# Kernel optimization log

Measured on AMD Instinct MI355X. Metric: run time of the kernel, lower is better.

The kernel has to match this reference:

```python
import jax, jax.numpy as jnp
import numpy as np

DIM = 288          # = C*9 patch features
RED = DIM // 2     # 144, reduced dim inside EffAttention
HEADS = 8
HD = RED // HEADS  # 18
SCALE = HD ** -0.5
NCHUNK = 4
EPS = 1e-5


def layer_norm(x, g, b):
    mu = jnp.mean(x, axis=-1, keepdims=True)
    var = jnp.mean(jnp.square(x - mu), axis=-1, keepdims=True)
    return (x - mu) * jax.lax.rsqrt(var + EPS) * g + b


def extract_patches_3x3(x):
    # x: [B, C, H, W] -> [B, C*9, H*W], same padding, stride 1.
    # Channel ordering matches torch.nn.Unfold: index = c*9 + ki*3 + kj.
    B, C, H, W = x.shape
    xp = jnp.pad(x, ((0, 0), (0, 0), (1, 1), (1, 1)))
    pats = jnp.stack([xp[:, :, i:i + H, j:j + W]
                      for i in range(3) for j in range(3)], axis=2)  # [B,C,9,H,W]
    return pats.reshape(B, C * 9, H * W)


def eff_attention(x, reduce_w, qkv_w, proj_w, proj_b):
    # x: [B, N, DIM]
    B, N, _ = x.shape
    h = x @ reduce_w                                   # [B, N, RED]
    qkv = (h @ qkv_w).reshape(B, N, 3, HEADS, HD)
    qkv = qkv.transpose(2, 0, 3, 1, 4)                 # [3, B, H, N, hd]
    q, k, v = qkv[0], qkv[1], qkv[2]
    chunk = N // NCHUNK
    q = q.reshape(B, HEADS, NCHUNK, chunk, HD)
    k = k.reshape(B, HEADS, NCHUNK, chunk, HD)
    v = v.reshape(B, HEADS, NCHUNK, chunk, HD)
    attn = jnp.einsum('bhcqd,bhckd->bhcqk', q, k) * SCALE
    attn = jax.nn.softmax(attn, axis=-1)
    out = jnp.einsum('bhcqk,bhckd->bhcqd', attn, v)    # [B,H,c,q,hd]
    out = out.transpose(0, 2, 3, 1, 4).reshape(B, N, RED)
    return out @ proj_w + proj_b


def setup_inputs() -> dict:
    key = jax.random.key(0)
    ks = jax.random.split(key, 12)
    s = 0.05
    return {
        'x': jax.random.normal(ks[0], (4, 32, 64, 64), jnp.float32),
        'norm1_g': jnp.ones((DIM,), jnp.float32),
        'norm1_b': jnp.zeros((DIM,), jnp.float32),
        'reduce_w': jax.random.normal(ks[1], (DIM, RED), jnp.float32) * s,
        'qkv_w': jax.random.normal(ks[2], (RED, 3 * RED), jnp.float32) * s,
        'proj_w': jax.random.normal(ks[3], (RED, DIM), jnp.float32) * s,
        'proj_b': jnp.zeros((DIM,), jnp.float32),
        'norm2_g': jnp.ones((DIM,), jnp.float32),
        'norm2_b': jnp.zeros((DIM,), jnp.float32),
        'fc1_w': jax.random.normal(ks[4], (DIM, DIM // 4), jnp.float32) * s,
        'fc1_b': jnp.zeros((DIM // 4,), jnp.float32),
        'fc2_w': jax.random.normal(ks[5], (DIM // 4, DIM), jnp.float32) * s,
        'fc2_b': jnp.zeros((DIM,), jnp.float32),
    }


def reference(x, norm1_g, norm1_b, reduce_w, qkv_w, proj_w, proj_b,
              norm2_g, norm2_b, fc1_w, fc1_b, fc2_w, fc2_b):
    t = extract_patches_3x3(x).transpose(0, 2, 1)      # [B, N, DIM]
    t = t + eff_attention(layer_norm(t, norm1_g, norm1_b),
                          reduce_w, qkv_w, proj_w, proj_b)
    h = layer_norm(t, norm2_g, norm2_b)
    h = jax.nn.relu(h @ fc1_w + fc1_b) @ fc2_w + fc2_b
    return t + h
```

## Files before the change

kernel.cpp:

```cpp
#include <hip/hip_runtime.h>
#include <hip/hip_bf16.h>

typedef __attribute__((ext_vector_type(4))) float f32x4;
typedef __attribute__((ext_vector_type(8))) short s16x8;
typedef __attribute__((ext_vector_type(2))) unsigned int u32x2;
typedef __attribute__((ext_vector_type(4))) unsigned int u32x4;
typedef unsigned short u16;
typedef unsigned int u32;

#define MTOT 16384
#define QSCALE 0.34004649151f

__device__ __forceinline__ u16 f2bf(float f){
  u32 u = __builtin_bit_cast(u32, f);
  u = (u + 0x7fffu + ((u >> 16) & 1u)) >> 16;
  return (u16)u;
}
__device__ __forceinline__ float bf2f(u16 u){
  u32 x = ((u32)u) << 16;
  return __builtin_bit_cast(float, x);
}
__device__ __forceinline__ float bfu32lo(u32 w){ return __builtin_bit_cast(float, (u32)(w << 16)); }
__device__ __forceinline__ float bfu32hi(u32 w){ return __builtin_bit_cast(float, (u32)(w & 0xffff0000u)); }
__device__ __forceinline__ u32 cvtpk(float lo, float hi){
  u32 r;
  asm("v_cvt_pk_bf16_f32 %0, %1, %2" : "=v"(r) : "v"(lo), "v"(hi));
  return r;
}
__device__ __forceinline__ float fexp2(float x){
  float r;
  asm("v_exp_f32 %0, %1" : "=v"(r) : "v"(x));
  return r;
}

__global__ __launch_bounds__(256) void head_k(
    const float* __restrict__ x, const float* __restrict__ g, const float* __restrict__ b_,
    u16* __restrict__ tb, u16* __restrict__ ln1,
    const float* __restrict__ rw, const float* __restrict__ qw,
    const float* __restrict__ pw, const float* __restrict__ f1, const float* __restrict__ f2,
    u16* __restrict__ WcT, u16* __restrict__ pwT, u16* __restrict__ f1wT, u16* __restrict__ f2wT)
{
  __shared__ float lds_t[32][296];
  __shared__ float red_s[8][32];
  __shared__ float red_q[8][32];
  __shared__ float smu[32], srs[32];
  int bid = blockIdx.x;
  int tid = threadIdx.x;
  if (bid >= 512){
    int idx = (bid - 512) * 256 + tid;
    const int N1 = 288*432, N2 = 288*160, N3 = 72*288;
    if (idx < N1){
      int i = idx / 432, j = idx - i * 432;
      float acc = 0.f;
      for (int k = 0; k < 144; ++k) acc += rw[i*144 + k] * qw[k*432 + j];
      WcT[j*288 + i] = f2bf(acc);
    } else if (idx < N1 + N2){
      int t = idx - N1; int n = t / 160, k = t - n * 160;
      pwT[t] = (k < 144) ? f2bf(pw[k*288 + n]) : (u16)0;
    } else if (idx < N1 + N2 + N3){
      int t = idx - (N1 + N2); int n = t / 288, k = t - n * 288;
      f1wT[t] = f2bf(f1[k*72 + n]);
    } else {
      int t = idx - (N1 + N2 + N3); int n = t / 96, k = t - n * 96;
      f2wT[t] = (k < 72) ? f2bf(f2[k*288 + n]) : (u16)0;
    }
    return;
  }
  int b = bid >> 7, i = (bid >> 1) & 63, j0 = (bid & 1) * 32;
  int q = tid >> 5;
  int jl = tid & 31;
  int j = j0 + jl;
  const float* xb = x + ((long)b * 32) * 4096;
  float s = 0.f, ss = 0.f;
#pragma unroll
  for (int c4 = 0; c4 < 4; ++c4){
    int c = q * 4 + c4;
    const float* xc = xb + c * 4096;
#pragma unroll
    for (int di = 0; di < 3; ++di){
      int ii = i + di - 1;
      bool iok = (ii >= 0) && (ii < 64);
#pragma unroll
      for (int dj = 0; dj < 3; ++dj){
        int jj = j + dj - 1;
        float v = 0.f;
        if (iok && jj >= 0 && jj < 64) v = xc[ii * 64 + jj];
        lds_t[jl][c * 9 + di * 3 + dj] = v;
        s += v; ss += v * v;
      }
    }
  }
  red_s[q][jl] = s; red_q[q][jl] = ss;
  __syncthreads();
  if (q == 0){
    float S = 0.f, SS = 0.f;
#pragma unroll
    for (int k = 0; k < 8; ++k){ S += red_s[k][jl]; SS += red_q[k][jl]; }
    float mu = S * (1.f/288.f);
    float var = SS * (1.f/288.f) - mu * mu;
    smu[jl] = mu;
    srs[jl] = rsqrtf(var + 1e-5f);
  }
  __syncthreads();
  long rowbase = ((long)b * 4096 + i * 64 + j0) * 288;
  for (int it = 0; it < 9; ++it){
    int idx = tid + it * 256;
    int p = idx / 72;
    int kk = idx - p * 72;
    f32x4 v = *(f32x4*)&lds_t[p][kk * 4];
    long base = rowbase + (long)p * 288 + kk * 4;
    u32x2 pt;
    pt[0] = (u32)f2bf(v[0]) | ((u32)f2bf(v[1]) << 16);
    pt[1] = (u32)f2bf(v[2]) | ((u32)f2bf(v[3]) << 16);
    *(u32x2*)&tb[base] = pt;
    float mu = smu[p], rs = srs[p];
    u16 o0 = f2bf((v[0]-mu)*rs*g[kk*4+0] + b_[kk*4+0]);
    u16 o1 = f2bf((v[1]-mu)*rs*g[kk*4+1] + b_[kk*4+1]);
    u16 o2 = f2bf((v[2]-mu)*rs*g[kk*4+2] + b_[kk*4+2]);
    u16 o3 = f2bf((v[3]-mu)*rs*g[kk*4+3] + b_[kk*4+3]);
    u32x2 pk;
    pk[0] = (u32)o0 | ((u32)o1 << 16);
    pk[1] = (u32)o2 | ((u32)o3 << 16);
    *(u32x2*)&ln1[base] = pk;
  }
}

template<int MODE, int KP, int MR>
__global__ __launch_bounds__(256) void gemm_k(
    const u16* __restrict__ A, const u16* __restrict__ BT,
    const float* __restrict__ bias, const void* __restrict__ resp,
    void* __restrict__ out0, void* __restrict__ out1, void* __restrict__ out2,
    int M, int N, int K)
{
  __shared__ u16 As[MR][KP + 8];
  __shared__ u16 Bs[64][KP + 8];
  const int nseg = KP >> 3;
  int tid = threadIdx.x;
  int m0 = blockIdx.x * MR, n0 = blockIdx.y * 64;
  for (int idx = tid; idx < (MR + 64) * nseg; idx += 256){
    int r = idx / nseg, sg = idx - r * nseg;
    if (r < MR){
      s16x8 v = {0,0,0,0,0,0,0,0};
      if (sg * 8 < K) v = *(const s16x8*)(A + (long)(m0 + r) * K + sg * 8);
      *(s16x8*)&As[r][sg * 8] = v;
    } else {
      int rb = r - MR;
      s16x8 w = {0,0,0,0,0,0,0,0};
      if (n0 + rb < N) w = *(const s16x8*)(BT + (long)(n0 + rb) * KP + sg * 8);
      *(s16x8*)&Bs[rb][sg * 8] = w;
    }
  }
  __syncthreads();
  int wv = tid >> 6, l = tid & 63;
  int lq = l & 15, lg = l >> 4;

#define EPI(ACC, MROW, NCOL) {                                           \
    int mrow = (MROW);                                                   \
    int ncol = (NCOL);                                                   \
    if (ncol < N){                                                       \
      if (MODE == 0){                                                    \
        int which = ncol / 144;                                          \
        int rem = ncol - which * 144;                                    \
        int hh = rem / 18;                                               \
        int dd = rem - hh * 18;                                          \
        _Pragma("unroll")                                                \
        for (int e = 0; e < 4; ++e){                                     \
          int row = mrow + e;                                            \
          long bch = (long)((row >> 10) * 8 + hh);                       \
          int kk = row & 1023;                                           \
          float v = ACC[e];                                              \
          if (which == 0){                                               \
            ((u16*)out0)[(bch<<15) + kk*32 + dd] = f2bf(v * QSCALE);     \
            if (dd < 14) ((u16*)out0)[(bch<<15) + kk*32 + 18 + dd] = (u16)0; \
          } else if (which == 1){                                        \
            int cp = (dd >> 3) ^ ((kk >> 1) & 3);                        \
            ((u16*)out1)[(bch<<15) + kk*32 + (cp<<3) + (dd&7)] = f2bf(v);\
          } else {                                                       \
            int seg = kk >> 8, jg = (kk >> 3) & 31, jp = jg ^ (dd & 7);  \
            ((u16*)out2)[(bch<<15) + seg*8192 + dd*256 + (jp<<3) + (kk&7)] = f2bf(v); \
            if (dd == 0){                                                \
              int jp1 = jg ^ 2;                                          \
              ((u16*)out2)[(bch<<15) + seg*8192 + 18*256 + (jp1<<3) + (kk&7)] = (u16)0x3F80; \
            }                                                            \
          }                                                              \
        }                                                                \
      } else {                                                           \
        float bv = bias[ncol];                                           \
        _Pragma("unroll")                                                \
        for (int e = 0; e < 4; ++e){                                     \
          long off = (long)(mrow + e) * N + ncol;                        \
          float v = ACC[e] + bv;                                         \
          if (MODE == 1){ v += bf2f(((const u16*)resp)[off]); ((u16*)out0)[off] = f2bf(v); } \
        }                                                                \
      }                                                                  \
    }                                                                    \
  }

  if constexpr (MR == 64){
    int wr = wv >> 1, wc = wv & 1;
    f32x4 acc00={0,0,0,0}, acc01={0,0,0,0}, acc10={0,0,0,0}, acc11={0,0,0,0};
    for (int kt = 0; kt < KP; kt += 32){
      s16x8 a0 = *(const s16x8*)&As[wr*32 + lq][kt + lg*8];
      s16x8 a1 = *(const s16x8*)&As[wr*32 + 16 + lq][kt + lg*8];
      s16x8 b0 = *(const s16x8*)&Bs[wc*32 + lq][kt + lg*8];
      s16x8 b1 = *(const s16x8*)&Bs[wc*32 + 16 + lq][kt + lg*8];
      acc00 = __builtin_amdgcn_mfma_f32_16x16x32_bf16(a0, b0, acc00, 0, 0, 0);
      acc01 = __builtin_amdgcn_mfma_f32_16x16x32_bf16(a0, b1, acc01, 0, 0, 0);
      acc10 = __builtin_amdgcn_mfma_f32_16x16x32_bf16(a1, b0, acc10, 0, 0, 0);
      acc11 = __builtin_amdgcn_mfma_f32_16x16x32_bf16(a1, b1, acc11, 0, 0, 0);
    }
    EPI(acc00, m0 + wr*32 + 0*16 + lg*4, n0 + wc*32 + 0*16 + lq)
    EPI(acc01, m0 + wr*32 + 0*16 + lg*4, n0 + wc*32 + 1*16 + lq)
    EPI(acc10, m0 + wr*32 + 1*16 + lg*4, n0 + wc*32 + 0*16 + lq)
    EPI(acc11, m0 + wr*32 + 1*16 + lg*4, n0 + wc*32 + 1*16 + lq)
  } else {
    f32x4 c00={0,0,0,0}, c01={0,0,0,0}, c02={0,0,0,0}, c03={0,0,0,0};
    f32x4 c10={0,0,0,0}, c11={0,0,0,0}, c12={0,0,0,0}, c13={0,0,0,0};
    for (int kt = 0; kt < KP; kt += 32){
      s16x8 a0 = *(const s16x8*)&As[wv*32 + lq][kt + lg*8];
      s16x8 a1 = *(const s16x8*)&As[wv*32 + 16 + lq][kt + lg*8];
      s16x8 b0 = *(const s16x8*)&Bs[ 0 + lq][kt + lg*8];
      s16x8 b1 = *(const s16x8*)&Bs[16 + lq][kt + lg*8];
      s16x8 b2 = *(const s16x8*)&Bs[32 + lq][kt + lg*8];
      s16x8 b3 = *(const s16x8*)&Bs[48 + lq][kt + lg*8];
      c00 = __builtin_amdgcn_mfma_f32_16x16x32_bf16(a0, b0, c00, 0, 0, 0);
      c01 = __builtin_amdgcn_mfma_f32_16x16x32_bf16(a0, b1, c01, 0, 0, 0);
      c02 = __builtin_amdgcn_mfma_f32_16x16x32_bf16(a0, b2, c02, 0, 0, 0);
      c03 = __builtin_amdgcn_mfma_f32_16x16x32_bf16(a0, b3, c03, 0, 0, 0);
      c10 = __builtin_amdgcn_mfma_f32_16x16x32_bf16(a1, b0, c10, 0, 0, 0);
      c11 = __builtin_amdgcn_mfma_f32_16x16x32_bf16(a1, b1, c11, 0, 0, 0);
      c12 = __builtin_amdgcn_mfma_f32_16x16x32_bf16(a1, b2, c12, 0, 0, 0);
      c13 = __builtin_amdgcn_mfma_f32_16x16x32_bf16(a1, b3, c13, 0, 0, 0);
    }
    EPI(c00, m0 + wv*32 + lg*4,      n0 +  0 + lq)
    EPI(c01, m0 + wv*32 + lg*4,      n0 + 16 + lq)
    EPI(c02, m0 + wv*32 + lg*4,      n0 + 32 + lq)
    EPI(c03, m0 + wv*32 + lg*4,      n0 + 48 + lq)
    EPI(c10, m0 + wv*32 + 16 + lg*4, n0 +  0 + lq)
    EPI(c11, m0 + wv*32 + 16 + lg*4, n0 + 16 + lq)
    EPI(c12, m0 + wv*32 + 16 + lg*4, n0 + 32 + lq)
    EPI(c13, m0 + wv*32 + 16 + lg*4, n0 + 48 + lq)
  }
#undef EPI
}

__global__ __launch_bounds__(256) void attn_k(
    const u16* __restrict__ Qp, const u16* __restrict__ Kpp,
    const u16* __restrict__ Vt, u16* __restrict__ ao)
{
  __shared__ u16 Ks[8192];
  __shared__ u16 Vs[8192];
  int bid = blockIdx.x;
  int qt = bid >> 7, bch = bid & 127;
  int b = bch >> 5, c = (bch >> 3) & 3, h = bch & 7;
  int tid = threadIdx.x, wv = tid >> 6, l = tid & 63;
  int lq = l & 15, lg = l >> 4;
  long base = (long)bch << 15;
  int q0 = qt * 256 + wv * 64 + lq;
  s16x8 qf0 = *(const s16x8*)(Qp + base + (long)(q0     ) * 32 + lg * 8);
  s16x8 qf1 = *(const s16x8*)(Qp + base + (long)(q0 + 16) * 32 + lg * 8);
  s16x8 qf2 = *(const s16x8*)(Qp + base + (long)(q0 + 32) * 32 + lg * 8);
  s16x8 qf3 = *(const s16x8*)(Qp + base + (long)(q0 + 48) * 32 + lg * 8);
  f32x4 oA0={0,0,0,0}, oA1={0,0,0,0}, oA2={0,0,0,0}, oA3={0,0,0,0};
  f32x4 oB0={0,0,0,0}, oB1={0,0,0,0}, oB2={0,0,0,0}, oB3={0,0,0,0};
  const f32x4 zf = {0,0,0,0};
  const u16* kg = Kpp + base;
  const u16* vg = Vt + base;
  u32x4 kr[4], vr[4];
#pragma unroll
  for (int r = 0; r < 4; ++r){
    kr[r] = *(const u32x4*)(kg + (r*256 + tid) * 8);
    vr[r] = *(const u32x4*)(vg + (r*256 + tid) * 8);
  }
  int kswz = (lq >> 1) & 3;
  int vswz = lq & 7;
  int ho = (lg & 1) << 2;
  int gl = lg >> 1;
  for (int seg = 0; seg < 4; ++seg){
    __syncthreads();
#pragma unroll
    for (int r = 0; r < 4; ++r){
      *(u32x4*)&Ks[(r*256 + tid) * 8] = kr[r];
      *(u32x4*)&Vs[(r*256 + tid) * 8] = vr[r];
    }
    __syncthreads();
    if (seg < 3){
      const u16* kgn = kg + (seg + 1) * 8192;
      const u16* vgn = vg + (seg + 1) * 8192;
#pragma unroll
      for (int r = 0; r < 4; ++r){
        kr[r] = *(const u32x4*)(kgn + (r*256 + tid) * 8);
        vr[r] = *(const u32x4*)(vgn + (r*256 + tid) * 8);
      }
    }
#pragma unroll 2
    for (int t32 = 0; t32 < 8; ++t32){
      int k0 = t32 * 32;
      int r0 = k0 + lq, r1 = k0 + 16 + lq;
      s16x8 kf0 = *(const s16x8*)&Ks[r0*32 + ((lg ^ kswz) << 3)];
      s16x8 kf1 = *(const s16x8*)&Ks[r1*32 + ((lg ^ kswz) << 3)];
      f32x4 s00 = __builtin_amdgcn_mfma_f32_16x16x32_bf16(kf0, qf0, zf, 0, 0, 0);
      f32x4 s01 = __builtin_amdgcn_mfma_f32_16x16x32_bf16(kf0, qf1, zf, 0, 0, 0);
      f32x4 s02 = __builtin_amdgcn_mfma_f32_16x16x32_bf16(kf0, qf2, zf, 0, 0, 0);
      f32x4 s03 = __builtin_amdgcn_mfma_f32_16x16x32_bf16(kf0, qf3, zf, 0, 0, 0);
      f32x4 s10 = __builtin_amdgcn_mfma_f32_16x16x32_bf16(kf1, qf0, zf, 0, 0, 0);
      f32x4 s11 = __builtin_amdgcn_mfma_f32_16x16x32_bf16(kf1, qf1, zf, 0, 0, 0);
      f32x4 s12 = __builtin_amdgcn_mfma_f32_16x16x32_bf16(kf1, qf2, zf, 0, 0, 0);
      f32x4 s13 = __builtin_amdgcn_mfma_f32_16x16x32_bf16(kf1, qf3, zf, 0, 0, 0);
      s16x8 pb0, pb1, pb2, pb3;
      {
        u32x4 w0, w1, w2, w3;
        w0[0] = cvtpk(fexp2(s00[0]), fexp2(s00[1]));
        w0[1] = cvtpk(fexp2(s00[2]), fexp2(s00[3]));
        w0[2] = cvtpk(fexp2(s10[0]), fexp2(s10[1]));
        w0[3] = cvtpk(fexp2(s10[2]), fexp2(s10[3]));
        w1[0] = cvtpk(fexp2(s01[0]), fexp2(s01[1]));
        w1[1] = cvtpk(fexp2(s01[2]), fexp2(s01[3]));
        w1[2] = cvtpk(fexp2(s11[0]), fexp2(s11[1]));
        w1[3] = cvtpk(fexp2(s11[2]), fexp2(s11[3]));
        w2[0] = cvtpk(fexp2(s02[0]), fexp2(s02[1]));
        w2[1] = cvtpk(fexp2(s02[2]), fexp2(s02[3]));
        w2[2] = cvtpk(fexp2(s12[0]), fexp2(s12[1]));
        w2[3] = cvtpk(fexp2(s12[2]), fexp2(s12[3]));
        w3[0] = cvtpk(fexp2(s03[0]), fexp2(s03[1]));
        w3[1] = cvtpk(fexp2(s03[2]), fexp2(s03[3]));
        w3[2] = cvtpk(fexp2(s13[0]), fexp2(s13[1]));
        w3[3] = cvtpk(fexp2(s13[2]), fexp2(s13[3]));
        pb0 = __builtin_bit_cast(s16x8, w0);
        pb1 = __builtin_bit_cast(s16x8, w1);
        pb2 = __builtin_bit_cast(s16x8, w2);
        pb3 = __builtin_bit_cast(s16x8, w3);
      }
      int G1 = (k0 >> 3) + gl;
      int a_lo = lq*256 + ((G1 ^ vswz) << 3) + ho;
      int a_hi = lq*256 + (((G1 + 2) ^ vswz) << 3) + ho;
      u32x2 vl0 = *(const u32x2*)&Vs[a_lo];
      u32x2 vh0 = *(const u32x2*)&Vs[a_hi];
      u32x2 vl1 = *(const u32x2*)&Vs[a_lo + 4096];
      u32x2 vh1 = *(const u32x2*)&Vs[a_hi + 4096];
      u32x4 vc0; vc0[0] = vl0[0]; vc0[1] = vl0[1]; vc0[2] = vh0[0]; vc0[3] = vh0[1];
      u32x4 vc1; vc1[0] = vl1[0]; vc1[1] = vl1[1]; vc1[2] = vh1[0]; vc1[3] = vh1[1];
      s16x8 va = __builtin_bit_cast(s16x8, vc0);
      s16x8 vb = __builtin_bit_cast(s16x8, vc1);
      oA0 = __builtin_amdgcn_mfma_f32_16x16x32_bf16(va, pb0, oA0, 0, 0, 0);
      oA1 = __builtin_amdgcn_mfma_f32_16x16x32_bf16(va, pb1, oA1, 0, 0, 0);
      oA2 = __builtin_amdgcn_mfma_f32_16x16x32_bf16(va, pb2, oA2, 0, 0, 0);
      oA3 = __builtin_amdgcn_mfma_f32_16x16x32_bf16(va, pb3, oA3, 0, 0, 0);
      oB0 = __builtin_amdgcn_mfma_f32_16x16x32_bf16(vb, pb0, oB0, 0, 0, 0);
      oB1 = __builtin_amdgcn_mfma_f32_16x16x32_bf16(vb, pb1, oB1, 0, 0, 0);
      oB2 = __builtin_amdgcn_mfma_f32_16x16x32_bf16(vb, pb2, oB2, 0, 0, 0);
      oB3 = __builtin_amdgcn_mfma_f32_16x16x32_bf16(vb, pb3, oB3, 0, 0, 0);
    }
  }
  long cn = (long)b * 4096 + c * 1024;
#define OUTJ(J, OA, OB) {                                                \
    float L = __shfl(OB[2], lq, 64);                                     \
    float rL = 1.f / L;                                                  \
    long ob = (cn + q0 + 16*(J)) * 144 + h * 18;                         \
    _Pragma("unroll")                                                    \
    for (int e = 0; e < 4; ++e)                                          \
      ao[ob + lg * 4 + e] = f2bf(OA[e] * rL);                            \
    if (lg == 0){                                                        \
      ao[ob + 16] = f2bf(OB[0] * rL);                                    \
      ao[ob + 17] = f2bf(OB[1] * rL);                                    \
    }                                                                    \
  }
  OUTJ(0, oA0, oB0)
  OUTJ(1, oA1, oB1)
  OUTJ(2, oA2, oB2)
  OUTJ(3, oA3, oB3)
#undef OUTJ
}

__global__ __launch_bounds__(256) void mlp_k(
    const u16* __restrict__ t2, const float* __restrict__ g, const float* __restrict__ b_,
    const u16* __restrict__ f1wT, const float* __restrict__ f1b,
    const u16* __restrict__ f2wT, const float* __restrict__ f2b,
    float* __restrict__ out)
{
  __shared__ u16 T2s[64][296];
  __shared__ u16 H1s[64][104];
  __shared__ float smu[64], srs[64];
  int tid = threadIdx.x;
  int wv = tid >> 6, l = tid & 63;
  int lq = l & 15, lg = l >> 4;
  long row0 = (long)blockIdx.x * 64;
  for (int idx = tid; idx < 64*36; idx += 256){
    int r = idx / 36, sg = idx - r*36;
    *(s16x8*)&T2s[r][sg*8] = *(const s16x8*)(t2 + (row0 + r)*288 + sg*8);
  }
  for (int idx = tid; idx < 64*16; idx += 256){
    int r = idx >> 4, c2 = idx & 15;
    *(u32*)&H1s[r][72 + c2*2] = 0u;
  }
  __syncthreads();
  {
    int r = tid >> 2, qt = tid & 3;
    const u16* pr = &T2s[r][qt*72];
    float s = 0.f, ss = 0.f;
#pragma unroll 4
    for (int i = 0; i < 36; ++i){
      u32 w = *(const u32*)(pr + i*2);
      float a = bfu32lo(w), c = bfu32hi(w);
      s += a + c; ss += a*a + c*c;
    }
    s  += __shfl_xor(s, 1, 64);  s  += __shfl_xor(s, 2, 64);
    ss += __shfl_xor(ss, 1, 64); ss += __shfl_xor(ss, 2, 64);
    if (qt == 0){
      float mu = s * (1.f/288.f);
      float var = ss * (1.f/288.f) - mu*mu;
      smu[r] = mu; srs[r] = rsqrtf(var + 1e-5f);
    }
  }
  __syncthreads();
  int myrow = wv*16 + lq;
  float mu = smu[myrow], rs = srs[myrow];
  f32x4 a0={0,0,0,0}, a1={0,0,0,0}, a2={0,0,0,0}, a3={0,0,0,0}, a4={0,0,0,0};
  int n4c = (lq < 8) ? (64 + lq) : 71;
#pragma unroll
  for (int kt = 0; kt < 9; ++kt){
    s16x8 raw = *(const s16x8*)&T2s[myrow][kt*32 + lg*8];
    f32x4 g0 = *(const f32x4*)(g  + kt*32 + lg*8);
    f32x4 g1 = *(const f32x4*)(g  + kt*32 + lg*8 + 4);
    f32x4 b0 = *(const f32x4*)(b_ + kt*32 + lg*8);
    f32x4 b1 = *(const f32x4*)(b_ + kt*32 + lg*8 + 4);
    s16x8 af;
#pragma unroll
    for (int i = 0; i < 4; ++i){
      af[i]   = (short)f2bf((bf2f((u16)raw[i])   - mu)*rs*g0[i] + b0[i]);
      af[4+i] = (short)f2bf((bf2f((u16)raw[4+i]) - mu)*rs*g1[i] + b1[i]);
    }
    s16x8 w0 = *(const s16x8*)(f1wT + (lq     )*288 + kt*32 + lg*8);
    s16x8 w1 = *(const s16x8*)(f1wT + (16 + lq)*288 + kt*32 + lg*8);
    s16x8 w2 = *(const s16x8*)(f1wT + (32 + lq)*288 + kt*32 + lg*8);
    s16x8 w3 = *(const s16x8*)(f1wT + (48 + lq)*288 + kt*32 + lg*8);
    s16x8 w4 = *(const s16x8*)(f1wT + (n4c    )*288 + kt*32 + lg*8);
    a0 = __builtin_amdgcn_mfma_f32_16x16x32_bf16(af, w0, a0, 0, 0, 0);
    a1 = __builtin_amdgcn_mfma_f32_16x16x32_bf16(af, w1, a1, 0, 0, 0);
    a2 = __builtin_amdgcn_mfma_f32_16x16x32_bf16(af, w2, a2, 0, 0, 0);
    a3 = __builtin_amdgcn_mfma_f32_16x16x32_bf16(af, w3, a3, 0, 0, 0);
    a4 = __builtin_amdgcn_mfma_f32_16x16x32_bf16(af, w4, a4, 0, 0, 0);
  }
#define H1W(ACC, F) { int n = (F)*16 + lq; if (n < 72){ float bv = f1b[n];        \
    _Pragma("unroll") for (int e = 0; e < 4; ++e)                                 \
      H1s[wv*16 + lg*4 + e][n] = f2bf(fmaxf(ACC[e] + bv, 0.f)); } }
  H1W(a0,0) H1W(a1,1) H1W(a2,2) H1W(a3,3) H1W(a4,4)
#undef H1W
  __syncthreads();
  f32x4 c[18];
#pragma unroll
  for (int f = 0; f < 18; ++f) c[f] = (f32x4){0,0,0,0};
#pragma unroll
  for (int kt = 0; kt < 3; ++kt){
    s16x8 af = *(const s16x8*)&H1s[myrow][kt*32 + lg*8];
#pragma unroll
    for (int f = 0; f < 18; ++f){
      s16x8 wf = *(const s16x8*)(f2wT + (f*16 + lq)*96 + kt*32 + lg*8);
      c[f] = __builtin_amdgcn_mfma_f32_16x16x32_bf16(af, wf, c[f], 0, 0, 0);
    }
  }
#pragma unroll
  for (int f = 0; f < 18; ++f){
    int col = f*16 + lq;
    float bv = f2b[col];
#pragma unroll
    for (int e = 0; e < 4; ++e){
      int rl = wv*16 + lg*4 + e;
      out[(row0 + rl)*288 + col] = c[f][e] + bv + bf2f(T2s[rl][col]);
    }
  }
}

extern "C" void kernel_launch(void* const* d_in, const int* in_sizes, int n_in,
                              void* d_out, int out_size, void* d_ws, size_t ws_size,
                              hipStream_t stream)
{
  const float* x   = (const float*)d_in[0];
  const float* n1g = (const float*)d_in[1];
  const float* n1b = (const float*)d_in[2];
  const float* rw  = (const float*)d_in[3];
  const float* qw  = (const float*)d_in[4];
  const float* pw  = (const float*)d_in[5];
  const float* pb  = (const float*)d_in[6];
  const float* n2g = (const float*)d_in[7];
  const float* n2b = (const float*)d_in[8];
  const float* f1w = (const float*)d_in[9];
  const float* f1b = (const float*)d_in[10];
  const float* f2w = (const float*)d_in[11];
  const float* f2b = (const float*)d_in[12];
  char* ws = (char*)d_ws;
  u16*   tb   = (u16*)(ws + 0);
  u16*   ln1b = (u16*)(ws + 9437184);
  u16*   Qp   = (u16*)(ws + 18874368);
  u16*   Kp   = (u16*)(ws + 27262976);
  u16*   Vtp  = (u16*)(ws + 35651584);
  u16*   aob  = (u16*)(ws + 44040192);
  u16*   t2   = (u16*)(ws + 18874368);
  u16*   WcT  = (u16*)(ws + 48758784);
  u16*   pwT  = (u16*)(ws + 49007616);
  u16*   f1wT = (u16*)(ws + 49099776);
  u16*   f2wT = (u16*)(ws + 49141248);
  float* out  = (float*)d_out;

  head_k<<<1367, 256, 0, stream>>>(x, n1g, n1b, tb, ln1b,
                                   rw, qw, pw, f1w, f2w, WcT, pwT, f1wT, f2wT);
  gemm_k<0,288,64><<<dim3(256,7), 256, 0, stream>>>(ln1b, WcT, nullptr, nullptr, Qp, Kp, Vtp, MTOT, 432, 288);
  attn_k<<<512, 256, 0, stream>>>(Qp, Kp, Vtp, aob);
  gemm_k<1,160,64><<<dim3(256,5), 256, 0, stream>>>(aob, pwT, pb, tb, t2, nullptr, nullptr, MTOT, 288, 144);
  mlp_k<<<256, 256, 0, stream>>>(t2, n2g, n2b, f1wT, f1b, f2wT, f2b, out);
}
```

Measured before the change: 122.8 us.

## Split attention keys across two blocks and add a combine kernel

Attention now launches twice as many blocks, each processing half of the key sequence per chunk, writing unnormalized partial outputs and row sums to workspace. A new combine kernel sums the two partials and divides by the total row sum. This aims to increase parallelism and latency hiding in attention, at the cost of an extra launch, extra global traffic and an extra bf16 rounding of partial results.

After: 128.9 us. 4.9% more time.

```diff
diff --git a/kernel.cpp b/kernel.cpp
--- a/kernel.cpp
+++ b/kernel.cpp
@@ -246,12 +246,15 @@
 
 __global__ __launch_bounds__(256) void attn_k(
     const u16* __restrict__ Qp, const u16* __restrict__ Kpp,
-    const u16* __restrict__ Vt, u16* __restrict__ ao)
+    const u16* __restrict__ Vt, u16* __restrict__ paoO0, u16* __restrict__ paoO1,
+    float* __restrict__ paoL)
 {
   __shared__ u16 Ks[8192];
   __shared__ u16 Vs[8192];
   int bid = blockIdx.x;
-  int qt = bid >> 7, bch = bid & 127;
+  int kh = bid >> 9;
+  int r2 = bid & 511;
+  int qt = r2 >> 7, bch = r2 & 127;
   int b = bch >> 5, c = (bch >> 3) & 3, h = bch & 7;
   int tid = threadIdx.x, wv = tid >> 6, l = tid & 63;
   int lq = l & 15, lg = l >> 4;
@@ -264,8 +267,8 @@
   f32x4 oA0={0,0,0,0}, oA1={0,0,0,0}, oA2={0,0,0,0}, oA3={0,0,0,0};
   f32x4 oB0={0,0,0,0}, oB1={0,0,0,0}, oB2={0,0,0,0}, oB3={0,0,0,0};
   const f32x4 zf = {0,0,0,0};
-  const u16* kg = Kpp + base;
-  const u16* vg = Vt + base;
+  const u16* kg = Kpp + base + kh * 16384;
+  const u16* vg = Vt  + base + kh * 16384;
   u32x4 kr[4], vr[4];
 #pragma unroll
   for (int r = 0; r < 4; ++r){
@@ -276,7 +279,7 @@
   int vswz = lq & 7;
   int ho = (lg & 1) << 2;
   int gl = lg >> 1;
-  for (int seg = 0; seg < 4; ++seg){
+  for (int sg2 = 0; sg2 < 2; ++sg2){
     __syncthreads();
 #pragma unroll
     for (int r = 0; r < 4; ++r){
@@ -284,9 +287,9 @@
       *(u32x4*)&Vs[(r*256 + tid) * 8] = vr[r];
     }
     __syncthreads();
-    if (seg < 3){
-      const u16* kgn = kg + (seg + 1) * 8192;
-      const u16* vgn = vg + (seg + 1) * 8192;
+    if (sg2 == 0){
+      const u16* kgn = kg + 8192;
+      const u16* vgn = vg + 8192;
 #pragma unroll
       for (int r = 0; r < 4; ++r){
         kr[r] = *(const u32x4*)(kgn + (r*256 + tid) * 8);
@@ -353,16 +356,18 @@
     }
   }
   long cn = (long)b * 4096 + c * 1024;
+  u16* po = kh ? paoO1 : paoO0;
+  float* pl = paoL + (long)kh * 131072;
 #define OUTJ(J, OA, OB) {                                                \
-    float L = __shfl(OB[2], lq, 64);                                     \
-    float rL = 1.f / L;                                                  \
-    long ob = (cn + q0 + 16*(J)) * 144 + h * 18;                         \
+    long row = cn + q0 + 16*(J);                                         \
+    long ob = row * 144 + h * 18;                                        \
     _Pragma("unroll")                                                    \
     for (int e = 0; e < 4; ++e)                                          \
-      ao[ob + lg * 4 + e] = f2bf(OA[e] * rL);                            \
+      po[ob + lg * 4 + e] = f2bf(OA[e]);                                 \
     if (lg == 0){                                                        \
-      ao[ob + 16] = f2bf(OB[0] * rL);                                    \
-      ao[ob + 17] = f2bf(OB[1] * rL);                                    \
+      po[ob + 16] = f2bf(OB[0]);                                         \
+      po[ob + 17] = f2bf(OB[1]);                                         \
+      pl[row * 8 + h] = OB[2];                                           \
     }                                                                    \
   }
   OUTJ(0, oA0, oB0)
@@ -370,6 +375,31 @@
   OUTJ(2, oA2, oB2)
   OUTJ(3, oA3, oB3)
 #undef OUTJ
+}
+
+__global__ __launch_bounds__(256) void comb_k(
+    u16* __restrict__ o0, const u16* __restrict__ o1, const float* __restrict__ paoL)
+{
+  int idx = blockIdx.x * 256 + threadIdx.x;
+  int row = idx / 18, sg = idx - row * 18;
+  const float* l0 = paoL + (long)row * 8;
+  const float* l1 = paoL + 131072 + (long)row * 8;
+  long off = (long)row * 144 + sg * 8;
+  u32x4 a = *(const u32x4*)(o0 + off);
+  u32x4 b = *(const u32x4*)(o1 + off);
+  int c0 = sg * 8;
+  u32x4 res;
+#pragma unroll
+  for (int w = 0; w < 4; ++w){
+    int cl = c0 + w*2, ch = cl + 1;
+    int hl = cl / 18, hh = ch / 18;
+    float rLl = 1.f / (l0[hl] + l1[hl]);
+    float rLh = 1.f / (l0[hh] + l1[hh]);
+    float sl = (bfu32lo(a[w]) + bfu32lo(b[w])) * rLl;
+    float sh = (bfu32hi(a[w]) + bfu32hi(b[w])) * rLh;
+    res[w] = (u32)f2bf(sl) | ((u32)f2bf(sh) << 16);
+  }
+  *(u32x4*)(o0 + off) = res;
 }
 
 __global__ __launch_bounds__(256) void mlp_k(
@@ -489,23 +519,27 @@
   const float* f2w = (const float*)d_in[11];
   const float* f2b = (const float*)d_in[12];
   char* ws = (char*)d_ws;
-  u16*   tb   = (u16*)(ws + 0);
-  u16*   ln1b = (u16*)(ws + 9437184);
-  u16*   Qp   = (u16*)(ws + 18874368);
-  u16*   Kp   = (u16*)(ws + 27262976);
-  u16*   Vtp  = (u16*)(ws + 35651584);
-  u16*   aob  = (u16*)(ws + 44040192);
-  u16*   t2   = (u16*)(ws + 18874368);
-  u16*   WcT  = (u16*)(ws + 48758784);
-  u16*   pwT  = (u16*)(ws + 49007616);
-  u16*   f1wT = (u16*)(ws + 49099776);
-  u16*   f2wT = (u16*)(ws + 49141248);
-  float* out  = (float*)d_out;
+  u16*   tb    = (u16*)(ws + 0);
+  u16*   ln1b  = (u16*)(ws + 9437184);
+  u16*   paoO0 = (u16*)(ws + 9437184);
+  float* paoL  = (float*)(ws + 14155776);
+  u16*   Qp    = (u16*)(ws + 18874368);
+  u16*   Kp    = (u16*)(ws + 27262976);
+  u16*   Vtp   = (u16*)(ws + 35651584);
+  u16*   paoO1 = (u16*)(ws + 44040192);
+  u16*   aob   = paoO0;
+  u16*   t2    = (u16*)(ws + 18874368);
+  u16*   WcT   = (u16*)(ws + 48758784);
+  u16*   pwT   = (u16*)(ws + 49007616);
+  u16*   f1wT  = (u16*)(ws + 49099776);
+  u16*   f2wT  = (u16*)(ws + 49141248);
+  float* out   = (float*)d_out;
 
   head_k<<<1367, 256, 0, stream>>>(x, n1g, n1b, tb, ln1b,
                                    rw, qw, pw, f1w, f2w, WcT, pwT, f1wT, f2wT);
   gemm_k<0,288,64><<<dim3(256,7), 256, 0, stream>>>(ln1b, WcT, nullptr, nullptr, Qp, Kp, Vtp, MTOT, 432, 288);
-  attn_k<<<512, 256, 0, stream>>>(Qp, Kp, Vtp, aob);
+  attn_k<<<1024, 256, 0, stream>>>(Qp, Kp, Vtp, paoO0, paoO1, paoL);
+  comb_k<<<1152, 256, 0, stream>>>(paoO0, paoO1, paoL);
   gemm_k<1,160,64><<<dim3(256,5), 256, 0, stream>>>(aob, pwT, pb, tb, t2, nullptr, nullptr, MTOT, 288, 144);
   mlp_k<<<256, 256, 0, stream>>>(t2, n2g, n2b, f1wT, f1b, f2wT, f2b, out);
 }
```

## Fuse output projection and residual into the MLP tail kernel

Applied to the files above, without the earlier changes.

Removes the separate projection GEMM launch and folds the attention output projection, bias and residual add into the MLP kernel. The new tail_k loads the attention output tile into LDS and computes the projection with MFMA, reading the projection weights directly from global memory. It writes the result into the T2s tile in place, so the t2 intermediate never makes a round trip through global memory. In exchange, each of the 256 blocks carries 18 accumulators and re-reads the projection weights per block, which raises register pressure and leaves only 256 blocks of parallelism for the projection. The gemm_k template loses its MODE 1 and MR=128 paths.

After: 113.5 us. -7.6%, faster.

```diff
diff --git a/kernel.cpp b/kernel.cpp
--- a/kernel.cpp
+++ b/kernel.cpp
@@ -158,45 +158,35 @@
     int mrow = (MROW);                                                   \
     int ncol = (NCOL);                                                   \
     if (ncol < N){                                                       \
-      if (MODE == 0){                                                    \
-        int which = ncol / 144;                                          \
-        int rem = ncol - which * 144;                                    \
-        int hh = rem / 18;                                               \
-        int dd = rem - hh * 18;                                          \
-        _Pragma("unroll")                                                \
-        for (int e = 0; e < 4; ++e){                                     \
-          int row = mrow + e;                                            \
-          long bch = (long)((row >> 10) * 8 + hh);                       \
-          int kk = row & 1023;                                           \
-          float v = ACC[e];                                              \
-          if (which == 0){                                               \
-            ((u16*)out0)[(bch<<15) + kk*32 + dd] = f2bf(v * QSCALE);     \
-            if (dd < 14) ((u16*)out0)[(bch<<15) + kk*32 + 18 + dd] = (u16)0; \
-          } else if (which == 1){                                        \
-            int cp = (dd >> 3) ^ ((kk >> 1) & 3);                        \
-            ((u16*)out1)[(bch<<15) + kk*32 + (cp<<3) + (dd&7)] = f2bf(v);\
-          } else {                                                       \
-            int seg = kk >> 8, jg = (kk >> 3) & 31, jp = jg ^ (dd & 7);  \
-            ((u16*)out2)[(bch<<15) + seg*8192 + dd*256 + (jp<<3) + (kk&7)] = f2bf(v); \
-            if (dd == 0){                                                \
-              int jp1 = jg ^ 2;                                          \
-              ((u16*)out2)[(bch<<15) + seg*8192 + 18*256 + (jp1<<3) + (kk&7)] = (u16)0x3F80; \
-            }                                                            \
+      int which = ncol / 144;                                            \
+      int rem = ncol - which * 144;                                      \
+      int hh = rem / 18;                                                 \
+      int dd = rem - hh * 18;                                            \
+      _Pragma("unroll")                                                  \
+      for (int e = 0; e < 4; ++e){                                       \
+        int row = mrow + e;                                              \
+        long bch = (long)((row >> 10) * 8 + hh);                         \
+        int kk = row & 1023;                                             \
+        float v = ACC[e];                                                \
+        if (which == 0){                                                 \
+          ((u16*)out0)[(bch<<15) + kk*32 + dd] = f2bf(v * QSCALE);       \
+          if (dd < 14) ((u16*)out0)[(bch<<15) + kk*32 + 18 + dd] = (u16)0; \
+        } else if (which == 1){                                          \
+          int cp = (dd >> 3) ^ ((kk >> 1) & 3);                          \
+          ((u16*)out1)[(bch<<15) + kk*32 + (cp<<3) + (dd&7)] = f2bf(v);  \
+        } else {                                                         \
+          int seg = kk >> 8, jg = (kk >> 3) & 31, jp = jg ^ (dd & 7);    \
+          ((u16*)out2)[(bch<<15) + seg*8192 + dd*256 + (jp<<3) + (kk&7)] = f2bf(v); \
+          if (dd == 0){                                                  \
+            int jp1 = jg ^ 2;                                            \
+            ((u16*)out2)[(bch<<15) + seg*8192 + 18*256 + (jp1<<3) + (kk&7)] = (u16)0x3F80; \
           }                                                              \
-        }                                                                \
-      } else {                                                           \
-        float bv = bias[ncol];                                           \
-        _Pragma("unroll")                                                \
-        for (int e = 0; e < 4; ++e){                                     \
-          long off = (long)(mrow + e) * N + ncol;                        \
-          float v = ACC[e] + bv;                                         \
-          if (MODE == 1){ v += bf2f(((const u16*)resp)[off]); ((u16*)out0)[off] = f2bf(v); } \
         }                                                                \
       }                                                                  \
     }                                                                    \
   }
 
-  if constexpr (MR == 64){
+  {
     int wr = wv >> 1, wc = wv & 1;
     f32x4 acc00={0,0,0,0}, acc01={0,0,0,0}, acc10={0,0,0,0}, acc11={0,0,0,0};
     for (int kt = 0; kt < KP; kt += 32){
@@ -213,33 +203,6 @@
     EPI(acc01, m0 + wr*32 + 0*16 + lg*4, n0 + wc*32 + 1*16 + lq)
     EPI(acc10, m0 + wr*32 + 1*16 + lg*4, n0 + wc*32 + 0*16 + lq)
     EPI(acc11, m0 + wr*32 + 1*16 + lg*4, n0 + wc*32 + 1*16 + lq)
-  } else {
-    f32x4 c00={0,0,0,0}, c01={0,0,0,0}, c02={0,0,0,0}, c03={0,0,0,0};
-    f32x4 c10={0,0,0,0}, c11={0,0,0,0}, c12={0,0,0,0}, c13={0,0,0,0};
-    for (int kt = 0; kt < KP; kt += 32){
-      s16x8 a0 = *(const s16x8*)&As[wv*32 + lq][kt + lg*8];
-      s16x8 a1 = *(const s16x8*)&As[wv*32 + 16 + lq][kt + lg*8];
-      s16x8 b0 = *(const s16x8*)&Bs[ 0 + lq][kt + lg*8];
-      s16x8 b1 = *(const s16x8*)&Bs[16 + lq][kt + lg*8];
-      s16x8 b2 = *(const s16x8*)&Bs[32 + lq][kt + lg*8];
-      s16x8 b3 = *(const s16x8*)&Bs[48 + lq][kt + lg*8];
-      c00 = __builtin_amdgcn_mfma_f32_16x16x32_bf16(a0, b0, c00, 0, 0, 0);
-      c01 = __builtin_amdgcn_mfma_f32_16x16x32_bf16(a0, b1, c01, 0, 0, 0);
-      c02 = __builtin_amdgcn_mfma_f32_16x16x32_bf16(a0, b2, c02, 0, 0, 0);
-      c03 = __builtin_amdgcn_mfma_f32_16x16x32_bf16(a0, b3, c03, 0, 0, 0);
-      c10 = __builtin_amdgcn_mfma_f32_16x16x32_bf16(a1, b0, c10, 0, 0, 0);
-      c11 = __builtin_amdgcn_mfma_f32_16x16x32_bf16(a1, b1, c11, 0, 0, 0);
-      c12 = __builtin_amdgcn_mfma_f32_16x16x32_bf16(a1, b2, c12, 0, 0, 0);
-      c13 = __builtin_amdgcn_mfma_f32_16x16x32_bf16(a1, b3, c13, 0, 0, 0);
-    }
-    EPI(c00, m0 + wv*32 + lg*4,      n0 +  0 + lq)
-    EPI(c01, m0 + wv*32 + lg*4,      n0 + 16 + lq)
-    EPI(c02, m0 + wv*32 + lg*4,      n0 + 32 + lq)
-    EPI(c03, m0 + wv*32 + lg*4,      n0 + 48 + lq)
-    EPI(c10, m0 + wv*32 + 16 + lg*4, n0 +  0 + lq)
-    EPI(c11, m0 + wv*32 + 16 + lg*4, n0 + 16 + lq)
-    EPI(c12, m0 + wv*32 + 16 + lg*4, n0 + 32 + lq)
-    EPI(c13, m0 + wv*32 + 16 + lg*4, n0 + 48 + lq)
   }
 #undef EPI
 }
@@ -372,12 +335,15 @@
 #undef OUTJ
 }
 
-__global__ __launch_bounds__(256) void mlp_k(
-    const u16* __restrict__ t2, const float* __restrict__ g, const float* __restrict__ b_,
+__global__ __launch_bounds__(256) void tail_k(
+    const u16* __restrict__ ao, const u16* __restrict__ pwT, const float* __restrict__ pbias,
+    const u16* __restrict__ tbp,
+    const float* __restrict__ g, const float* __restrict__ b_,
     const u16* __restrict__ f1wT, const float* __restrict__ f1b,
     const u16* __restrict__ f2wT, const float* __restrict__ f2b,
     float* __restrict__ out)
 {
+  __shared__ u16 AOs[64][168];
   __shared__ u16 T2s[64][296];
   __shared__ u16 H1s[64][104];
   __shared__ float smu[64], srs[64];
@@ -385,13 +351,45 @@
   int wv = tid >> 6, l = tid & 63;
   int lq = l & 15, lg = l >> 4;
   long row0 = (long)blockIdx.x * 64;
+  for (int idx = tid; idx < 64*20; idx += 256){
+    int r = idx / 20, sg = idx - r*20;
+    s16x8 v = {0,0,0,0,0,0,0,0};
+    if (sg < 18) v = *(const s16x8*)(ao + (row0 + r)*144 + sg*8);
+    *(s16x8*)&AOs[r][sg*8] = v;
+  }
   for (int idx = tid; idx < 64*36; idx += 256){
     int r = idx / 36, sg = idx - r*36;
-    *(s16x8*)&T2s[r][sg*8] = *(const s16x8*)(t2 + (row0 + r)*288 + sg*8);
+    *(s16x8*)&T2s[r][sg*8] = *(const s16x8*)(tbp + (row0 + r)*288 + sg*8);
   }
   for (int idx = tid; idx < 64*16; idx += 256){
     int r = idx >> 4, c2 = idx & 15;
     *(u32*)&H1s[r][72 + c2*2] = 0u;
+  }
+  __syncthreads();
+  {
+    f32x4 c[18];
+#pragma unroll
+    for (int f = 0; f < 18; ++f) c[f] = (f32x4){0,0,0,0};
+#pragma unroll
+    for (int kt = 0; kt < 5; ++kt){
+      s16x8 af = *(const s16x8*)&AOs[wv*16 + lq][kt*32 + lg*8];
+#pragma unroll
+      for (int f = 0; f < 18; ++f){
+        s16x8 wf = *(const s16x8*)(pwT + (long)(f*16 + lq)*160 + kt*32 + lg*8);
+        c[f] = __builtin_amdgcn_mfma_f32_16x16x32_bf16(af, wf, c[f], 0, 0, 0);
+      }
+    }
+#pragma unroll
+    for (int f = 0; f < 18; ++f){
+      int col = f*16 + lq;
+      float bv = pbias[col];
+#pragma unroll
+      for (int e = 0; e < 4; ++e){
+        int rl = wv*16 + lg*4 + e;
+        float v = c[f][e] + bv + bf2f(T2s[rl][col]);
+        T2s[rl][col] = f2bf(v);
+      }
+    }
   }
   __syncthreads();
   {
@@ -495,7 +493,6 @@
   u16*   Kp   = (u16*)(ws + 27262976);
   u16*   Vtp  = (u16*)(ws + 35651584);
   u16*   aob  = (u16*)(ws + 44040192);
-  u16*   t2   = (u16*)(ws + 18874368);
   u16*   WcT  = (u16*)(ws + 48758784);
   u16*   pwT  = (u16*)(ws + 49007616);
   u16*   f1wT = (u16*)(ws + 49099776);
@@ -506,6 +503,5 @@
                                    rw, qw, pw, f1w, f2w, WcT, pwT, f1wT, f2wT);
   gemm_k<0,288,64><<<dim3(256,7), 256, 0, stream>>>(ln1b, WcT, nullptr, nullptr, Qp, Kp, Vtp, MTOT, 432, 288);
   attn_k<<<512, 256, 0, stream>>>(Qp, Kp, Vtp, aob);
-  gemm_k<1,160,64><<<dim3(256,5), 256, 0, stream>>>(aob, pwT, pb, tb, t2, nullptr, nullptr, MTOT, 288, 144);
-  mlp_k<<<256, 256, 0, stream>>>(t2, n2g, n2b, f1wT, f1b, f2wT, f2b, out);
-}
+  tail_k<<<256, 256, 0, stream>>>(aob, pwT, pb, tb, n2g, n2b, f1wT, f1b, f2wT, f2b, out);
+}
```
